# Performance work log

Hardware: AMD Instinct MI355X
Metric: run time of the kernel (lower is better)

The kernel has to match this reference:

```python
import jax, jax.numpy as jnp
import numpy as np

C = 8            # feat_channel
B, K, H, W = 8, 32, 128, 128
CW = (C + 2) * C + C + C * C + C + C + 1  # 169


def setup_inputs() -> dict:
    key = jax.random.key(0)
    k1, k2, k3, k4, k5 = jax.random.split(key, 5)
    seg_feat = jax.random.normal(k1, (B, C, H, W), jnp.float32)
    conv_weight = jax.random.normal(k2, (B, CW, H, W), jnp.float32) * 0.1
    mask = jax.random.randint(k3, (B, K), 0, 2).astype(jnp.int32)
    ind = jax.random.randint(k4, (B, K), 0, H * W).astype(jnp.int64)
    target = jax.random.uniform(k5, (B, K, H, W), jnp.float32)
    return {"seg_feat": seg_feat, "conv_weight": conv_weight, "mask": mask,
            "ind": ind, "target": target}


def reference(seg_feat, conv_weight, mask, ind, target):
    b, c, h, w = seg_feat.shape
    k = ind.shape[1]
    # gather_feature(conv_weight, ind, use_transform=True): [B,CW,H,W] -> [B,HW,CW] -> gather -> [B,K,CW]
    cw = conv_weight.reshape(b, -1, h * w).transpose(0, 2, 1)
    weight = jnp.take_along_axis(cw, ind[:, :, None], axis=1)  # [B,K,CW]

    sizes = [(c + 2) * c, c, c * c, c, c, 1]
    splits = np.cumsum(sizes)[:-1]
    c1w, c1b, c2w, c2b, c3w, c3b = jnp.split(weight, splits, axis=-1)
    c1w = c1w.reshape(b, k, c, c + 2)   # per-object 1x1 conv weights
    c2w = c2w.reshape(b, k, c, c)
    c3w = c3w.reshape(b, k, 1, c)

    x = (ind % w).astype(jnp.float32)
    y = (ind // w).astype(jnp.float32)
    y_grid, x_grid = jnp.meshgrid(jnp.arange(h, dtype=jnp.float32),
                                  jnp.arange(w, dtype=jnp.float32), indexing='ij')
    x_rel = (x_grid[None, None] - x[:, :, None, None]) / w   # [B,K,H,W]
    y_rel = (y_grid[None, None] - y[:, :, None, None]) / h

    feat = jnp.concatenate([
        jnp.broadcast_to(seg_feat[:, None], (b, k, c, h, w)),
        x_rel[:, :, None], y_rel[:, :, None]], axis=2)       # [B,K,C+2,H,W]

    feat = jax.nn.relu(jnp.einsum('bkoc,bkchw->bkohw', c1w, feat) + c1b[..., None, None])
    feat = jax.nn.relu(jnp.einsum('bkoc,bkchw->bkohw', c2w, feat) + c2b[..., None, None])
    pred = jax.nn.sigmoid(jnp.einsum('bkoc,bkchw->bkohw', c3w, feat)
                          + c3b[..., None, None])[:, :, 0]    # [B,K,H,W]

    m = mask.astype(jnp.float32)[:, :, None, None]
    p = pred * m
    t = target * m
    smooth = 1.0
    inter = jnp.sum(p * t, axis=(1, 2, 3))
    denom = jnp.sum(p * p, axis=(1, 2, 3)) + jnp.sum(t * t, axis=(1, 2, 3)) + smooth
    per_img = 1.0 - (2.0 * inter + smooth) / denom
    return jnp.mean(per_img)   # sum over images / valid_batch_size (all valid)
```

## Files before the change

kernel.cpp:

```cpp
#include <hip/hip_runtime.h>

#define C8     8
#define KOBJ   32
#define BIMG   8
#define WW     128
#define HH     128
#define HWPIX  16384
#define CWN    169
#define PIX    8
#define GRIDX  8
#define NBLK_PER_B (KOBJ * GRIDX)


__global__ __launch_bounds__(256) void mask_head_kernel(
    const float* __restrict__ seg_feat,
    const float* __restrict__ conv_weight,
    const int* __restrict__ mask,
    const long long* __restrict__ ind,
    const float* __restrict__ target,
    float* __restrict__ partial)
{
    const int b    = blockIdx.z;
    const int k    = blockIdx.y;
    const int tile = blockIdx.x;
    const int t    = threadIdx.x;
    const int blockFlat = (b * KOBJ + k) * GRIDX + tile;
    float* my = partial + blockFlat * 3;

    if (mask[b * KOBJ + k] == 0) {
        if (t == 0) { my[0] = 0.f; my[1] = 0.f; my[2] = 0.f; }
        return;
    }

    __shared__ __align__(16) float l1w[C8][12];
    __shared__ __align__(16) float l2w[C8][C8];
    __shared__ __align__(16) float l1b[C8];
    __shared__ __align__(16) float l2b[C8];
    __shared__ __align__(16) float l3w[C8];
    __shared__ float l3b_s;
    __shared__ float red[4][3];

    const int idx = (int)ind[b * KOBJ + k];
    if (t < CWN) {
        const float v = conv_weight[(b * CWN + t) * HWPIX + idx];
        if (t < 80)       { l1w[t / 10][t % 10] = v; }
        else if (t < 88)  { l1b[t - 80] = v; }
        else if (t < 152) { const int u = t - 88; l2w[u >> 3][u & 7] = v; }
        else if (t < 160) { l2b[t - 152] = v; }
        else if (t < 168) { l3w[t - 160] = v; }
        else              { l3b_s = v; }
    }
    __syncthreads();

    const float cx = (float)(idx & (WW - 1));
    const float cy = (float)(idx >> 7);

    const float* seg = seg_feat + b * C8 * HWPIX;
    const float* tgt = target + (b * KOBJ + k) * HWPIX;

    const int p0 = (tile * 256 + t) * PIX;

    const float4 t4a = *reinterpret_cast<const float4*>(&tgt[p0]);
    const float4 t4b = *reinterpret_cast<const float4*>(&tgt[p0 + 4]);

    const float sy  = ((float)(p0 >> 7) - cy) * (1.0f / 128.0f);
    const float sx0 = ((float)(p0 & (WW - 1)) - cx) * (1.0f / 128.0f);
    float sx[PIX];
#pragma unroll
    for (int i = 0; i < PIX; ++i) sx[i] = sx0 + (float)i * (1.0f / 128.0f);

    float f[C8][PIX];
#pragma unroll
    for (int c = 0; c < C8; ++c) {
        const float4 a = *reinterpret_cast<const float4*>(&seg[c * HWPIX + p0]);
        const float4 d = *reinterpret_cast<const float4*>(&seg[c * HWPIX + p0 + 4]);
        f[c][0] = a.x; f[c][1] = a.y; f[c][2] = a.z; f[c][3] = a.w;
        f[c][4] = d.x; f[c][5] = d.y; f[c][6] = d.z; f[c][7] = d.w;
    }

    float h1[C8][PIX];
#pragma unroll
    for (int o = 0; o < C8; ++o) {
        const float4 wa = *reinterpret_cast<const float4*>(&l1w[o][0]);
        const float4 wb = *reinterpret_cast<const float4*>(&l1w[o][4]);
        const float4 wc = *reinterpret_cast<const float4*>(&l1w[o][8]);
        const float base = fmaf(wc.y, sy, l1b[o]);
#pragma unroll
        for (int i = 0; i < PIX; ++i) {
            float a = fmaf(wc.x, sx[i], base);
            a = fmaf(wa.x, f[0][i], a);
            a = fmaf(wa.y, f[1][i], a);
            a = fmaf(wa.z, f[2][i], a);
            a = fmaf(wa.w, f[3][i], a);
            a = fmaf(wb.x, f[4][i], a);
            a = fmaf(wb.y, f[5][i], a);
            a = fmaf(wb.z, f[6][i], a);
            a = fmaf(wb.w, f[7][i], a);
            h1[o][i] = fmaxf(a, 0.f);
        }
    }

    float h2[C8][PIX];
#pragma unroll
    for (int o = 0; o < C8; ++o) {
        const float4 wa = *reinterpret_cast<const float4*>(&l2w[o][0]);
        const float4 wb = *reinterpret_cast<const float4*>(&l2w[o][4]);
        const float bias = l2b[o];
#pragma unroll
        for (int i = 0; i < PIX; ++i) {
            float a = bias;
            a = fmaf(wa.x, h1[0][i], a);
            a = fmaf(wa.y, h1[1][i], a);
            a = fmaf(wa.z, h1[2][i], a);
            a = fmaf(wa.w, h1[3][i], a);
            a = fmaf(wb.x, h1[4][i], a);
            a = fmaf(wb.y, h1[5][i], a);
            a = fmaf(wb.z, h1[6][i], a);
            a = fmaf(wb.w, h1[7][i], a);
            h2[o][i] = fmaxf(a, 0.f);
        }
    }

    const float4 wa = *reinterpret_cast<const float4*>(&l3w[0]);
    const float4 wb = *reinterpret_cast<const float4*>(&l3w[4]);
    const float b3 = l3b_s;
    float tv[PIX];
    tv[0] = t4a.x; tv[1] = t4a.y; tv[2] = t4a.z; tv[3] = t4a.w;
    tv[4] = t4b.x; tv[5] = t4b.y; tv[6] = t4b.z; tv[7] = t4b.w;

    float s_pt = 0.f, s_pp = 0.f, s_tt = 0.f;
#pragma unroll
    for (int i = 0; i < PIX; ++i) {
        float z = b3;
        z = fmaf(wa.x, h2[0][i], z);
        z = fmaf(wa.y, h2[1][i], z);
        z = fmaf(wa.z, h2[2][i], z);
        z = fmaf(wa.w, h2[3][i], z);
        z = fmaf(wb.x, h2[4][i], z);
        z = fmaf(wb.y, h2[5][i], z);
        z = fmaf(wb.z, h2[6][i], z);
        z = fmaf(wb.w, h2[7][i], z);
        const float e    = __expf(-z);
        const float pred = __builtin_amdgcn_rcpf(1.0f + e);
        s_pt = fmaf(pred, tv[i], s_pt);
        s_pp = fmaf(pred, pred, s_pp);
        s_tt = fmaf(tv[i], tv[i], s_tt);
    }

#pragma unroll
    for (int off = 32; off > 0; off >>= 1) {
        s_pt += __shfl_down(s_pt, off);
        s_pp += __shfl_down(s_pp, off);
        s_tt += __shfl_down(s_tt, off);
    }
    const int wid = t >> 6;
    if ((t & 63) == 0) { red[wid][0] = s_pt; red[wid][1] = s_pp; red[wid][2] = s_tt; }
    __syncthreads();
    if (t == 0) {
        float a = 0.f, b2 = 0.f, c2 = 0.f;
#pragma unroll
        for (int i = 0; i < 4; ++i) { a += red[i][0]; b2 += red[i][1]; c2 += red[i][2]; }
        my[0] = a; my[1] = b2; my[2] = c2;
    }
}

__global__ __launch_bounds__(512) void finalize_kernel(
    const float* __restrict__ partial, float* __restrict__ out)
{
    const int t    = threadIdx.x;
    const int b    = t >> 6;
    const int lane = t & 63;

    float pt = 0.f, pp = 0.f, tt = 0.f;
    for (int e = lane; e < NBLK_PER_B; e += 64) {
        const float* q = partial + (b * NBLK_PER_B + e) * 3;
        pt += q[0]; pp += q[1]; tt += q[2];
    }
#pragma unroll
    for (int off = 32; off > 0; off >>= 1) {
        pt += __shfl_down(pt, off);
        pp += __shfl_down(pp, off);
        tt += __shfl_down(tt, off);
    }
    __shared__ float per[BIMG];
    if (lane == 0) {
        per[b] = 1.0f - (2.0f * pt + 1.0f) / (pp + tt + 1.0f);
    }
    __syncthreads();
    if (t == 0) {
        float s = 0.f;
#pragma unroll
        for (int i = 0; i < BIMG; ++i) s += per[i];
        out[0] = s * (1.0f / (float)BIMG);
    }
}

extern "C" void kernel_launch(void* const* d_in, const int* in_sizes, int n_in,
                              void* d_out, int out_size, void* d_ws, size_t ws_size,
                              hipStream_t stream) {
    const float*     seg  = (const float*)d_in[0];
    const float*     cw   = (const float*)d_in[1];
    const int*       mask = (const int*)d_in[2];
    const long long* ind  = (const long long*)d_in[3];
    const float*     tgt  = (const float*)d_in[4];
    float* out     = (float*)d_out;
    float* partial = (float*)d_ws;

    dim3 grid(GRIDX, KOBJ, BIMG);
    mask_head_kernel<<<grid, 256, 0, stream>>>(seg, cw, mask, ind, tgt, partial);
    finalize_kernel<<<1, 512, 0, stream>>>(partial, out);
}
```

Baseline: 19.73 us.

## Fuse finalize into main kernel via last-block atomic counter; fuse layer 2/3

Removes the separate finalize kernel launch: each block bumps a global atomic counter after writing its partials, and the last block to finish reduces all partials and writes the output. A memset of the counter is added on the stream. Layer 3 is also folded into the layer-2 loop so the h2 array is never materialized, which lowers register pressure. The cost is an atomic plus a thread fence per block, a serialized tail reduction in a single block, and an extra memset operation.

```diff
diff --git a/kernel.cpp b/kernel.cpp
--- a/kernel.cpp
+++ b/kernel.cpp
@@ -4,12 +4,12 @@
 #define KOBJ   32
 #define BIMG   8
 #define WW     128
-#define HH     128
 #define HWPIX  16384
 #define CWN    169
 #define PIX    8
 #define GRIDX  8
-#define NBLK_PER_B (KOBJ * GRIDX)
+#define SLOTS_PER_B (KOBJ * GRIDX)
+#define NBLK   (BIMG * SLOTS_PER_B)
 
 
 __global__ __launch_bounds__(256) void mask_head_kernel(
@@ -18,173 +18,176 @@
     const int* __restrict__ mask,
     const long long* __restrict__ ind,
     const float* __restrict__ target,
-    float* __restrict__ partial)
+    float* __restrict__ partial,
+    unsigned int* __restrict__ counter,
+    float* __restrict__ out)
 {
+    const int tile = blockIdx.x;
+    const int k    = blockIdx.y;
     const int b    = blockIdx.z;
-    const int k    = blockIdx.y;
-    const int tile = blockIdx.x;
     const int t    = threadIdx.x;
     const int blockFlat = (b * KOBJ + k) * GRIDX + tile;
     float* my = partial + blockFlat * 3;
 
-    if (mask[b * KOBJ + k] == 0) {
-        if (t == 0) { my[0] = 0.f; my[1] = 0.f; my[2] = 0.f; }
-        return;
-    }
-
     __shared__ __align__(16) float l1w[C8][12];
+    __shared__ __align__(16) float l1b[C8];
     __shared__ __align__(16) float l2w[C8][C8];
-    __shared__ __align__(16) float l1b[C8];
     __shared__ __align__(16) float l2b[C8];
     __shared__ __align__(16) float l3w[C8];
     __shared__ float l3b_s;
     __shared__ float red[4][3];
-
-    const int idx = (int)ind[b * KOBJ + k];
-    if (t < CWN) {
-        const float v = conv_weight[(b * CWN + t) * HWPIX + idx];
-        if (t < 80)       { l1w[t / 10][t % 10] = v; }
-        else if (t < 88)  { l1b[t - 80] = v; }
-        else if (t < 152) { const int u = t - 88; l2w[u >> 3][u & 7] = v; }
-        else if (t < 160) { l2b[t - 152] = v; }
-        else if (t < 168) { l3w[t - 160] = v; }
-        else              { l3b_s = v; }
+    __shared__ bool amLast;
+
+    const bool active = (mask[b * KOBJ + k] != 0);
+
+    if (active) {
+        const int idx = (int)ind[b * KOBJ + k];
+        if (t < CWN) {
+            const float v = conv_weight[(b * CWN + t) * HWPIX + idx];
+            if (t < 80)       { l1w[t / 10][t % 10] = v; }
+            else if (t < 88)  { l1b[t - 80] = v; }
+            else if (t < 152) { const int u = t - 88; l2w[u >> 3][u & 7] = v; }
+            else if (t < 160) { l2b[t - 152] = v; }
+            else if (t < 168) { l3w[t - 160] = v; }
+            else              { l3b_s = v; }
+        }
+        __syncthreads();
+
+        const float cx = (float)(idx & (WW - 1));
+        const float cy = (float)(idx >> 7);
+
+        const float* seg = seg_feat + b * C8 * HWPIX;
+        const float* tgt = target + (b * KOBJ + k) * HWPIX;
+
+        const int p0 = (tile * 256 + t) * PIX;
+
+        const float4 t4a = *reinterpret_cast<const float4*>(&tgt[p0]);
+        const float4 t4b = *reinterpret_cast<const float4*>(&tgt[p0 + 4]);
+
+        const float sy  = ((float)(p0 >> 7) - cy) * (1.0f / 128.0f);
+        const float sx0 = ((float)(p0 & (WW - 1)) - cx) * (1.0f / 128.0f);
+        float sx[PIX];
+#pragma unroll
+        for (int i = 0; i < PIX; ++i) sx[i] = sx0 + (float)i * (1.0f / 128.0f);
+
+        float f[C8][PIX];
+#pragma unroll
+        for (int c = 0; c < C8; ++c) {
+            const float4 a = *reinterpret_cast<const float4*>(&seg[c * HWPIX + p0]);
+            const float4 d = *reinterpret_cast<const float4*>(&seg[c * HWPIX + p0 + 4]);
+            f[c][0] = a.x; f[c][1] = a.y; f[c][2] = a.z; f[c][3] = a.w;
+            f[c][4] = d.x; f[c][5] = d.y; f[c][6] = d.z; f[c][7] = d.w;
+        }
+
+        float h1[C8][PIX];
+#pragma unroll
+        for (int o = 0; o < C8; ++o) {
+            const float4 wa = *reinterpret_cast<const float4*>(&l1w[o][0]);
+            const float4 wb = *reinterpret_cast<const float4*>(&l1w[o][4]);
+            const float4 wc = *reinterpret_cast<const float4*>(&l1w[o][8]);
+            const float base = fmaf(wc.y, sy, l1b[o]);
+#pragma unroll
+            for (int i = 0; i < PIX; ++i) {
+                float a = fmaf(wc.x, sx[i], base);
+                a = fmaf(wa.x, f[0][i], a);
+                a = fmaf(wa.y, f[1][i], a);
+                a = fmaf(wa.z, f[2][i], a);
+                a = fmaf(wa.w, f[3][i], a);
+                a = fmaf(wb.x, f[4][i], a);
+                a = fmaf(wb.y, f[5][i], a);
+                a = fmaf(wb.z, f[6][i], a);
+                a = fmaf(wb.w, f[7][i], a);
+                h1[o][i] = fmaxf(a, 0.f);
+            }
+        }
+
+        float z[PIX];
+        {
+            const float b3 = l3b_s;
+#pragma unroll
+            for (int i = 0; i < PIX; ++i) z[i] = b3;
+        }
+#pragma unroll
+        for (int o = 0; o < C8; ++o) {
+            const float4 wa = *reinterpret_cast<const float4*>(&l2w[o][0]);
+            const float4 wb = *reinterpret_cast<const float4*>(&l2w[o][4]);
+            const float bias = l2b[o];
+            const float w3 = l3w[o];
+#pragma unroll
+            for (int i = 0; i < PIX; ++i) {
+                float a = bias;
+                a = fmaf(wa.x, h1[0][i], a);
+                a = fmaf(wa.y, h1[1][i], a);
+                a = fmaf(wa.z, h1[2][i], a);
+                a = fmaf(wa.w, h1[3][i], a);
+                a = fmaf(wb.x, h1[4][i], a);
+                a = fmaf(wb.y, h1[5][i], a);
+                a = fmaf(wb.z, h1[6][i], a);
+                a = fmaf(wb.w, h1[7][i], a);
+                z[i] = fmaf(w3, fmaxf(a, 0.f), z[i]);
+            }
+        }
+
+        float tv[PIX];
+        tv[0] = t4a.x; tv[1] = t4a.y; tv[2] = t4a.z; tv[3] = t4a.w;
+        tv[4] = t4b.x; tv[5] = t4b.y; tv[6] = t4b.z; tv[7] = t4b.w;
+
+        float s_pt = 0.f, s_pp = 0.f, s_tt = 0.f;
+#pragma unroll
+        for (int i = 0; i < PIX; ++i) {
+            const float e    = __expf(-z[i]);
+            const float pred = __builtin_amdgcn_rcpf(1.0f + e);
+            s_pt = fmaf(pred, tv[i], s_pt);
+            s_pp = fmaf(pred, pred, s_pp);
+            s_tt = fmaf(tv[i], tv[i], s_tt);
+        }
+
+#pragma unroll
+        for (int off = 32; off > 0; off >>= 1) {
+            s_pt += __shfl_down(s_pt, off);
+            s_pp += __shfl_down(s_pp, off);
+            s_tt += __shfl_down(s_tt, off);
+        }
+        const int wid = t >> 6;
+        if ((t & 63) == 0) { red[wid][0] = s_pt; red[wid][1] = s_pp; red[wid][2] = s_tt; }
+        __syncthreads();
+        if (t == 0) {
+            float a = 0.f, b2 = 0.f, c2 = 0.f;
+#pragma unroll
+            for (int i = 0; i < 4; ++i) { a += red[i][0]; b2 += red[i][1]; c2 += red[i][2]; }
+            my[0] = a; my[1] = b2; my[2] = c2;
+        }
+    } else {
+        if (t == 0) { my[0] = 0.f; my[1] = 0.f; my[2] = 0.f; }
+    }
+
+    if (t == 0) {
+        __threadfence();
+        const unsigned prev = atomicAdd(counter, 1u);
+        amLast = (prev == (unsigned)(NBLK - 1));
     }
     __syncthreads();
-
-    const float cx = (float)(idx & (WW - 1));
-    const float cy = (float)(idx >> 7);
-
-    const float* seg = seg_feat + b * C8 * HWPIX;
-    const float* tgt = target + (b * KOBJ + k) * HWPIX;
-
-    const int p0 = (tile * 256 + t) * PIX;
-
-    const float4 t4a = *reinterpret_cast<const float4*>(&tgt[p0]);
-    const float4 t4b = *reinterpret_cast<const float4*>(&tgt[p0 + 4]);
-
-    const float sy  = ((float)(p0 >> 7) - cy) * (1.0f / 128.0f);
-    const float sx0 = ((float)(p0 & (WW - 1)) - cx) * (1.0f / 128.0f);
-    float sx[PIX];
-#pragma unroll
-    for (int i = 0; i < PIX; ++i) sx[i] = sx0 + (float)i * (1.0f / 128.0f);
-
-    float f[C8][PIX];
-#pragma unroll
-    for (int c = 0; c < C8; ++c) {
-        const float4 a = *reinterpret_cast<const float4*>(&seg[c * HWPIX + p0]);
-        const float4 d = *reinterpret_cast<const float4*>(&seg[c * HWPIX + p0 + 4]);
-        f[c][0] = a.x; f[c][1] = a.y; f[c][2] = a.z; f[c][3] = a.w;
-        f[c][4] = d.x; f[c][5] = d.y; f[c][6] = d.z; f[c][7] = d.w;
-    }
-
-    float h1[C8][PIX];
-#pragma unroll
-    for (int o = 0; o < C8; ++o) {
-        const float4 wa = *reinterpret_cast<const float4*>(&l1w[o][0]);
-        const float4 wb = *reinterpret_cast<const float4*>(&l1w[o][4]);
-        const float4 wc = *reinterpret_cast<const float4*>(&l1w[o][8]);
-        const float base = fmaf(wc.y, sy, l1b[o]);
-#pragma unroll
-        for (int i = 0; i < PIX; ++i) {
-            float a = fmaf(wc.x, sx[i], base);
-            a = fmaf(wa.x, f[0][i], a);
-            a = fmaf(wa.y, f[1][i], a);
-            a = fmaf(wa.z, f[2][i], a);
-            a = fmaf(wa.w, f[3][i], a);
-            a = fmaf(wb.x, f[4][i], a);
-            a = fmaf(wb.y, f[5][i], a);
-            a = fmaf(wb.z, f[6][i], a);
-            a = fmaf(wb.w, f[7][i], a);
-            h1[o][i] = fmaxf(a, 0.f);
-        }
-    }
-
-    float h2[C8][PIX];
-#pragma unroll
-    for (int o = 0; o < C8; ++o) {
-        const float4 wa = *reinterpret_cast<const float4*>(&l2w[o][0]);
-        const float4 wb = *reinterpret_cast<const float4*>(&l2w[o][4]);
-        const float bias = l2b[o];
-#pragma unroll
-        for (int i = 0; i < PIX; ++i) {
-            float a = bias;
-            a = fmaf(wa.x, h1[0][i], a);
-            a = fmaf(wa.y, h1[1][i], a);
-            a = fmaf(wa.z, h1[2][i], a);
-            a = fmaf(wa.w, h1[3][i], a);
-            a = fmaf(wb.x, h1[4][i], a);
-            a = fmaf(wb.y, h1[5][i], a);
-            a = fmaf(wb.z, h1[6][i], a);
-            a = fmaf(wb.w, h1[7][i], a);
-            h2[o][i] = fmaxf(a, 0.f);
-        }
-    }
-
-    const float4 wa = *reinterpret_cast<const float4*>(&l3w[0]);
-    const float4 wb = *reinterpret_cast<const float4*>(&l3w[4]);
-    const float b3 = l3b_s;
-    float tv[PIX];
-    tv[0] = t4a.x; tv[1] = t4a.y; tv[2] = t4a.z; tv[3] = t4a.w;
-    tv[4] = t4b.x; tv[5] = t4b.y; tv[6] = t4b.z; tv[7] = t4b.w;
-
-    float s_pt = 0.f, s_pp = 0.f, s_tt = 0.f;
-#pragma unroll
-    for (int i = 0; i < PIX; ++i) {
-        float z = b3;
-        z = fmaf(wa.x, h2[0][i], z);
-        z = fmaf(wa.y, h2[1][i], z);
-        z = fmaf(wa.z, h2[2][i], z);
-        z = fmaf(wa.w, h2[3][i], z);
-        z = fmaf(wb.x, h2[4][i], z);
-        z = fmaf(wb.y, h2[5][i], z);
-        z = fmaf(wb.z, h2[6][i], z);
-        z = fmaf(wb.w, h2[7][i], z);
-        const float e    = __expf(-z);
-        const float pred = __builtin_amdgcn_rcpf(1.0f + e);
-        s_pt = fmaf(pred, tv[i], s_pt);
-        s_pp = fmaf(pred, pred, s_pp);
-        s_tt = fmaf(tv[i], tv[i], s_tt);
-    }
-
-#pragma unroll
-    for (int off = 32; off > 0; off >>= 1) {
-        s_pt += __shfl_down(s_pt, off);
-        s_pp += __shfl_down(s_pp, off);
-        s_tt += __shfl_down(s_tt, off);
-    }
-    const int wid = t >> 6;
-    if ((t & 63) == 0) { red[wid][0] = s_pt; red[wid][1] = s_pp; red[wid][2] = s_tt; }
-    __syncthreads();
-    if (t == 0) {
-        float a = 0.f, b2 = 0.f, c2 = 0.f;
-#pragma unroll
-        for (int i = 0; i < 4; ++i) { a += red[i][0]; b2 += red[i][1]; c2 += red[i][2]; }
-        my[0] = a; my[1] = b2; my[2] = c2;
-    }
-}
-
-__global__ __launch_bounds__(512) void finalize_kernel(
-    const float* __restrict__ partial, float* __restrict__ out)
-{
-    const int t    = threadIdx.x;
-    const int b    = t >> 6;
+    if (!amLast) return;
+    __threadfence();
+
+    const int w    = t >> 6;
     const int lane = t & 63;
-
-    float pt = 0.f, pp = 0.f, tt = 0.f;
-    for (int e = lane; e < NBLK_PER_B; e += 64) {
-        const float* q = partial + (b * NBLK_PER_B + e) * 3;
-        pt += q[0]; pp += q[1]; tt += q[2];
-    }
-#pragma unroll
-    for (int off = 32; off > 0; off >>= 1) {
-        pt += __shfl_down(pt, off);
-        pp += __shfl_down(pp, off);
-        tt += __shfl_down(tt, off);
-    }
     __shared__ float per[BIMG];
-    if (lane == 0) {
-        per[b] = 1.0f - (2.0f * pt + 1.0f) / (pp + tt + 1.0f);
+    for (int img = w; img < BIMG; img += 4) {
+        const float* base = partial + img * SLOTS_PER_B * 3;
+        float pt = 0.f, pp = 0.f, tt = 0.f;
+        for (int s = lane; s < SLOTS_PER_B; s += 64) {
+            pt += base[s * 3 + 0];
+            pp += base[s * 3 + 1];
+            tt += base[s * 3 + 2];
+        }
+#pragma unroll
+        for (int off = 32; off > 0; off >>= 1) {
+            pt += __shfl_down(pt, off);
+            pp += __shfl_down(pp, off);
+            tt += __shfl_down(tt, off);
+        }
+        if (lane == 0) per[img] = 1.0f - (2.0f * pt + 1.0f) / (pp + tt + 1.0f);
     }
     __syncthreads();
     if (t == 0) {
@@ -203,10 +206,12 @@
     const int*       mask = (const int*)d_in[2];
     const long long* ind  = (const long long*)d_in[3];
     const float*     tgt  = (const float*)d_in[4];
-    float* out     = (float*)d_out;
-    float* partial = (float*)d_ws;
-
-    dim3 grid(GRIDX, KOBJ, BIMG);
-    mask_head_kernel<<<grid, 256, 0, stream>>>(seg, cw, mask, ind, tgt, partial);
-    finalize_kernel<<<1, 512, 0, stream>>>(partial, out);
+    float* out = (float*)d_out;
+
+    unsigned int* counter = (unsigned int*)d_ws;
+    float* partial = (float*)((char*)d_ws + 16);
+
+    hipMemsetAsync(counter, 0, sizeof(unsigned int), stream);
+    mask_head_kernel<<<dim3(GRIDX, KOBJ, BIMG), 256, 0, stream>>>(
+        seg, cw, mask, ind, tgt, partial, counter, out);
 }
```

Measured after the change: 60.85 us. 3.08x slower.
